# Performance work log

Hardware: AMD Instinct MI355X
Metric: run time of the kernel (lower is better)

The kernel has to match this reference:

```python
import jax, jax.numpy as jnp
import numpy as np

B, L, HID, NH = 1, 2048, 3072, 24
HD = HID // NH          # 128
MLP = HID * 4           # 12288


def _layernorm(x, eps=1e-6):
    # LayerNorm without affine (pre_norm)
    mu = jnp.mean(x, axis=-1, keepdims=True)
    var = jnp.mean(jnp.square(x - mu), axis=-1, keepdims=True)
    return (x - mu) * jax.lax.rsqrt(var + eps)


def _rmsnorm(x, w):
    # torch.nn.RMSNorm with eps=None -> finfo(dtype).eps
    eps = jnp.finfo(x.dtype).eps
    ms = jnp.mean(jnp.square(x), axis=-1, keepdims=True)
    return x * jax.lax.rsqrt(ms + eps) * w


def _apply_rope(x, pe):
    # x: (B, L, H, D); pe: (B, 1, L, D//2, 2, 2)
    b, l, h, d = x.shape
    x_ = x.astype(jnp.float32).reshape(b, l, h, d // 2, 1, 2)
    f = pe[:, :, :, None]                       # (B,1,L,1,D//2,2,2)
    out = f[..., 0] * x_[..., 0] + f[..., 1] * x_[..., 1]
    return out.reshape(b, l, h, d).astype(x.dtype)


def setup_inputs() -> dict:
    key = jax.random.key(0)
    ks = jax.random.split(key, 16)
    s = 0.02
    # pe as proper 2x2 rotation matrices (EmbedND output structure)
    theta = jax.random.uniform(ks[0], (L, HD // 2), minval=0.0, maxval=2.0 * np.pi)
    cos, sin = jnp.cos(theta), jnp.sin(theta)
    rot = jnp.stack([jnp.stack([cos, -sin], -1), jnp.stack([sin, cos], -1)], -2)
    pe = rot[None, None].astype(jnp.float32)    # (1,1,L,HD//2,2,2)
    rnd = lambda k, shp: jax.random.normal(k, shp, jnp.float32)
    return {
        "x": rnd(ks[1], (B, L, HID)),
        "vec": rnd(ks[2], (B, HID)),
        "pe": pe,
        "w_mod": rnd(ks[3], (HID, 3 * HID)) * s,
        "b_mod": rnd(ks[4], (3 * HID,)) * s,
        "w_qkv": rnd(ks[5], (HID, 3 * HID)) * s,
        "b_qkv": rnd(ks[6], (3 * HID,)) * s,
        "w_fc1": rnd(ks[7], (HID, MLP)) * s,
        "b_fc1": rnd(ks[8], (MLP,)) * s,
        "w_fc2": rnd(ks[9], (MLP, HID)) * s,
        "b_fc2": rnd(ks[10], (HID,)) * s,
        "w_out": rnd(ks[11], (HID, HID)) * s,
        "b_out": rnd(ks[12], (HID,)) * s,
        "norm_q_w": jnp.ones((HD,), jnp.float32),
        "norm_k_w": jnp.ones((HD,), jnp.float32),
    }


def reference(x, vec, pe, w_mod, b_mod, w_qkv, b_qkv, w_fc1, b_fc1,
              w_fc2, b_fc2, w_out, b_out, norm_q_w, norm_k_w):
    # modulation: AWQ linear on silu(vec)
    mod = jax.nn.silu(vec) @ w_mod + b_mod            # (B, 3*HID)
    shift, scale, gate = jnp.split(mod[:, None, :], 3, axis=-1)
    x_mod = _layernorm(x) * (1.0 + scale) + shift      # (B, L, HID)

    # qkv projection (SVDQ linear, dequantized math == dense GEMM)
    qkv = x_mod @ w_qkv + b_qkv
    q, k, v = jnp.split(qkv, 3, axis=-1)
    q = _rmsnorm(q.reshape(B, L, NH, HD), norm_q_w)
    k = _rmsnorm(k.reshape(B, L, NH, HD), norm_k_w)
    q = _apply_rope(q, pe)
    k = _apply_rope(k, pe)
    v = v.reshape(B, L, NH, HD)

    # scaled dot-product attention
    scores = jnp.einsum("blhd,bmhd->bhlm", q, k) / jnp.sqrt(jnp.float32(HD))
    probs = jax.nn.softmax(scores, axis=-1)
    attn = jnp.einsum("bhlm,bmhd->blhd", probs, v).reshape(B, L, HID)

    # parallel MLP branch
    mlp = jax.nn.gelu(x_mod @ w_fc1 + b_fc1, approximate=True)
    mlp = mlp @ w_fc2 + b_fc2

    out = attn @ w_out + b_out + mlp
    return x + gate * out
```

## Files before the change

### kernel.cpp

```cpp
#include <hip/hip_runtime.h>
#include <hip/hip_bf16.h>
#include <stdint.h>


typedef __bf16 bf16;
typedef bf16 bf16x2 __attribute__((ext_vector_type(2)));
typedef bf16 bf16x4 __attribute__((ext_vector_type(4)));
typedef bf16 bf16x8 __attribute__((ext_vector_type(8)));
typedef float f32x4 __attribute__((ext_vector_type(4)));

#define L_SEQ 2048
#define HIDD  3072
#define NHH   24
#define HDD   128
#define MLPD  12288
#define N3Q   9216

struct PB { bf16* p[8]; };

__device__ __forceinline__ void gload_lds16(const bf16* g, bf16* l) {
  __builtin_amdgcn_global_load_lds(
      (const __attribute__((address_space(1))) unsigned int*)g,
      (__attribute__((address_space(3))) unsigned int*)l, 16, 0, 0);
}

__device__ __forceinline__ float gelu_tanh(float x) {
  float z = 0.7978845608028654f * (x + 0.044715f * x * x * x);
  float t = 1.f - 2.f / (__expf(2.f * z) + 1.f);
  return 0.5f * x * (1.f + t);
}

__global__ __launch_bounds__(256) void mod_partial(
    const float* __restrict__ vec, const float* __restrict__ w_mod,
    float* __restrict__ part) {
  __shared__ float sv[256];
  int y = blockIdx.y;
  int i0 = y * 256;
  {
    float xv = vec[i0 + threadIdx.x];
    sv[threadIdx.x] = xv / (1.f + __expf(-xv));
  }
  __syncthreads();
  int j = blockIdx.x * 256 + threadIdx.x;
  float acc = 0.f;
#pragma unroll 8
  for (int i = 0; i < 256; ++i)
    acc += sv[i] * w_mod[(size_t)(i0 + i) * N3Q + j];
  part[y * N3Q + j] = acc;
}

__global__ __launch_bounds__(256) void mod_reduce(
    const float* __restrict__ part, const float* __restrict__ b_mod,
    float* __restrict__ mod) {
  int j = blockIdx.x * 256 + threadIdx.x;
  float s = b_mod[j];
#pragma unroll
  for (int p = 0; p < 12; ++p) s += part[p * N3Q + j];
  mod[j] = s;
}

__global__ __launch_bounds__(256) void ln_mod_k(
    const float* __restrict__ x, const float* __restrict__ mod,
    bf16* __restrict__ xm) {
  __shared__ float sb[4];
  int l = blockIdx.x, t = threadIdx.x;
  const float* xr = x + (size_t)l * HIDD;
  float4 v[3];
  float s = 0.f;
#pragma unroll
  for (int p = 0; p < 3; ++p) {
    v[p] = *(const float4*)(xr + p * 1024 + t * 4);
    s += v[p].x + v[p].y + v[p].z + v[p].w;
  }
#pragma unroll
  for (int o = 32; o >= 1; o >>= 1) s += __shfl_xor(s, o);
  if (!(t & 63)) sb[t >> 6] = s;
  __syncthreads();
  float mean = (sb[0] + sb[1] + sb[2] + sb[3]) * (1.f / HIDD);
  __syncthreads();
  float vs = 0.f;
#pragma unroll
  for (int p = 0; p < 3; ++p) {
    float a = v[p].x - mean, b = v[p].y - mean, c = v[p].z - mean,
          d = v[p].w - mean;
    vs += a * a + b * b + c * c + d * d;
  }
#pragma unroll
  for (int o = 32; o >= 1; o >>= 1) vs += __shfl_xor(vs, o);
  if (!(t & 63)) sb[t >> 6] = vs;
  __syncthreads();
  float var = (sb[0] + sb[1] + sb[2] + sb[3]) * (1.f / HIDD);
  float rs = rsqrtf(var + 1e-6f);
#pragma unroll
  for (int p = 0; p < 3; ++p) {
    int j = p * 1024 + t * 4;
    float4 sc = *(const float4*)(mod + HIDD + j);
    float4 sh = *(const float4*)(mod + j);
    bf16x4 o;
    o[0] = (bf16)((v[p].x - mean) * rs * (1.f + sc.x) + sh.x);
    o[1] = (bf16)((v[p].y - mean) * rs * (1.f + sc.y) + sh.y);
    o[2] = (bf16)((v[p].z - mean) * rs * (1.f + sc.z) + sh.z);
    o[3] = (bf16)((v[p].w - mean) * rs * (1.f + sc.w) + sh.w);
    *(bf16x4*)(xm + (size_t)l * HIDD + j) = o;
  }
}

__global__ __launch_bounds__(256) void convT(
    const float* __restrict__ src, bf16* __restrict__ dst, int K, int N) {
  __shared__ bf16 tl[64 * 72];
  int n0 = blockIdx.x * 64, k0 = blockIdx.y * 64;
  int t = threadIdx.x;
#pragma unroll
  for (int p = 0; p < 4; ++p) {
    int idx = p * 256 + t;
    int kr = idx >> 4, c4 = (idx & 15) << 2;
    float4 v = *(const float4*)(src + (size_t)(k0 + kr) * N + n0 + c4);
    bf16x4 b;
    b[0] = (bf16)v.x; b[1] = (bf16)v.y; b[2] = (bf16)v.z; b[3] = (bf16)v.w;
    *(bf16x4*)(tl + kr * 72 + c4) = b;
  }
  __syncthreads();
#pragma unroll
  for (int p = 0; p < 2; ++p) {
    int idx = p * 256 + t;
    int nr = idx >> 3, c = idx & 7;
    bf16x8 o;
#pragma unroll
    for (int j = 0; j < 8; ++j) o[j] = tl[(c * 8 + j) * 72 + nr];
    *(bf16x8*)(dst + (size_t)(n0 + nr) * K + k0 + c * 8) = o;
  }
}

template <int EPI>
__global__ __launch_bounds__(512, 2) void gemm256(
    const bf16* __restrict__ A, const bf16* __restrict__ BT,
    const float* __restrict__ bias, int lda, int klen, int ldc, PB dst,
    bf16* __restrict__ o1) {
  __shared__ bf16 LA[2][2][8192];
  __shared__ bf16 LB[2][2][8192];
  const int tid = threadIdx.x;
  const int w = tid >> 6, lane = tid & 63;
  const int wm = w >> 2, wn = w & 3;
  const int g = lane >> 4, r16 = lane & 15;
  const int row0 = blockIdx.x * 256, col0 = blockIdx.y * 256;
  const size_t kb = (size_t)blockIdx.z * klen;

  const int s_r = tid >> 3, s_c = tid & 7;
  const bf16* gA = A + (size_t)(row0 + s_r) * lda + kb + ((s_c ^ (s_r & 7)) << 3);
  const bf16* gB = BT + (size_t)(col0 + s_r) * lda + kb + ((s_c ^ (s_r & 7)) << 3);
  const int wofs = w * 512;

#define STG_A(buf, h, t)                                                       \
  do {                                                                         \
    gload_lds16(gA + (size_t)((h) * 128) * lda + (t) * 64, &LA[buf][h][wofs]); \
    gload_lds16(gA + (size_t)((h) * 128 + 64) * lda + (t) * 64,                \
                &LA[buf][h][4096 + wofs]);                                     \
  } while (0)
#define STG_B(buf, h, t)                                                       \
  do {                                                                         \
    gload_lds16(gB + (size_t)((h) * 128) * lda + (t) * 64, &LB[buf][h][wofs]); \
    gload_lds16(gB + (size_t)((h) * 128 + 64) * lda + (t) * 64,                \
                &LB[buf][h][4096 + wofs]);                                     \
  } while (0)
#define LGKM0()                                               \
  do {                                                        \
    asm volatile("s_waitcnt lgkmcnt(0)" ::: "memory");        \
    __builtin_amdgcn_sched_barrier(0);                        \
  } while (0)
#define MF(mb, AF, BF)                                                     \
  do {                                                                     \
    __builtin_amdgcn_s_setprio(1);                                         \
    _Pragma("unroll") for (int m_ = 0; m_ < 4; ++m_)                       \
        _Pragma("unroll") for (int n_ = 0; n_ < 4; ++n_)                   \
            acc[(mb) + m_][n_] = __builtin_amdgcn_mfma_f32_16x16x32_bf16(  \
                AF[(mb) + m_], BF[n_], acc[(mb) + m_][n_], 0, 0, 0);       \
    __builtin_amdgcn_s_setprio(0);                                         \
  } while (0)

  f32x4 acc[8][4] = {};
  const int nk = klen >> 6;
  const int swz0 = (g ^ (r16 & 7)) << 3;
  const int swz1 = ((4 + g) ^ (r16 & 7)) << 3;
  const int brow = (wn & 1) * 64;
  const int hb = wn >> 1;

  STG_A(0, 0, 0); STG_A(0, 1, 0); STG_B(0, 0, 0); STG_B(0, 1, 0);
  STG_B(1, 0, 1); STG_A(1, 0, 1); STG_A(1, 1, 1);
  asm volatile("s_waitcnt vmcnt(6)" ::: "memory");
  __builtin_amdgcn_s_barrier();

  for (int t = 0; t < nk; ++t) {
    const int buf = t & 1;
    const bf16* la = LA[buf][wm];
    const bf16* lb = LB[buf][hb];
    bf16x8 af0[8], af1[8], bf0[4], bf1[4];

#pragma unroll
    for (int m = 0; m < 8; ++m)
      af0[m] = *(const bf16x8*)(la + (m * 16 + r16) * 64 + swz0);
#pragma unroll
    for (int n = 0; n < 4; ++n)
      bf0[n] = *(const bf16x8*)(lb + (brow + n * 16 + r16) * 64 + swz0);
    __builtin_amdgcn_s_barrier();
    LGKM0();
    if (t + 1 < nk) STG_B(buf ^ 1, 1, t + 1);
    MF(0, af0, bf0);
    __builtin_amdgcn_s_barrier();

#pragma unroll
    for (int n = 0; n < 4; ++n)
      bf1[n] = *(const bf16x8*)(lb + (brow + n * 16 + r16) * 64 + swz1);
    __builtin_amdgcn_s_barrier();
    LGKM0();
    if (t + 2 < nk) STG_B(buf, 0, t + 2);
    MF(4, af0, bf0);
    __builtin_amdgcn_s_barrier();

#pragma unroll
    for (int m = 0; m < 4; ++m)
      af1[m] = *(const bf16x8*)(la + (m * 16 + r16) * 64 + swz1);
    __builtin_amdgcn_s_barrier();
    LGKM0();
    MF(0, af1, bf1);
    __builtin_amdgcn_s_barrier();

#pragma unroll
    for (int m = 4; m < 8; ++m)
      af1[m] = *(const bf16x8*)(la + (m * 16 + r16) * 64 + swz1);
    __builtin_amdgcn_s_barrier();
    LGKM0();
    if (t + 2 < nk) { STG_A(buf, 0, t + 2); STG_A(buf, 1, t + 2); }
    if (t < nk - 2) {
      asm volatile("s_waitcnt vmcnt(6)" ::: "memory");
    } else if (t == nk - 2) {
      asm volatile("s_waitcnt vmcnt(0)" ::: "memory");
    }
    MF(4, af1, bf1);
    __builtin_amdgcn_s_barrier();
  }
#undef STG_A
#undef STG_B
#undef LGKM0
#undef MF

  bf16* dp = (EPI == 0) ? dst.p[blockIdx.z] : o1;
#pragma unroll
  for (int m = 0; m < 8; ++m) {
    int row = row0 + wm * 128 + m * 16 + g * 4;
#pragma unroll
    for (int n = 0; n < 4; ++n) {
      int col = col0 + wn * 64 + n * 16 + r16;
      float bv = (EPI == 1) ? bias[col] : 0.f;
#pragma unroll
      for (int r = 0; r < 4; ++r) {
        float v = acc[m][n][r] + bv;
        if (EPI == 1) v = gelu_tanh(v);
        dp[(size_t)(row + r) * ldc + col] = (bf16)v;
      }
    }
  }
}

__global__ __launch_bounds__(256) void qknorm_rope_k(
    const bf16* __restrict__ P0, const bf16* __restrict__ P1,
    const float* __restrict__ b_qkv, const float* __restrict__ pe,
    const float* __restrict__ qw, const float* __restrict__ kw,
    bf16* __restrict__ qb, bf16* __restrict__ kb) {
  int t = threadIdx.x, lane = t & 63, w = t >> 6;
  int pair = blockIdx.x * 4 + w;
  int h = pair % NHH, l = pair / NHH;
  size_t qi = (size_t)l * N3Q + h * HDD + 2 * lane;
  size_t ob = (size_t)l * HIDD + h * HDD + 2 * lane;
  float4 f = *(const float4*)(pe + (size_t)l * 256 + lane * 4);
  float2 wq = *(const float2*)(qw + 2 * lane);
  float2 wk = *(const float2*)(kw + 2 * lane);
  {
    bf16x2 a = *(const bf16x2*)(P0 + qi);
    bf16x2 b = *(const bf16x2*)(P1 + qi);
    float2 bq = *(const float2*)(b_qkv + h * HDD + 2 * lane);
    float x0 = (float)a[0] + (float)b[0] + bq.x;
    float x1 = (float)a[1] + (float)b[1] + bq.y;
    float ss = x0 * x0 + x1 * x1;
#pragma unroll
    for (int o = 32; o >= 1; o >>= 1) ss += __shfl_xor(ss, o);
    float rs = rsqrtf(ss * (1.f / HDD) + 1.1920929e-7f);
    x0 *= rs * wq.x; x1 *= rs * wq.y;
    const float qs = 0.08838834764831845f;
    bf16x2 ov;
    ov[0] = (bf16)((f.x * x0 + f.y * x1) * qs);
    ov[1] = (bf16)((f.z * x0 + f.w * x1) * qs);
    *(bf16x2*)(qb + ob) = ov;
  }
  {
    bf16x2 a = *(const bf16x2*)(P0 + qi + HIDD);
    bf16x2 b = *(const bf16x2*)(P1 + qi + HIDD);
    float2 bk = *(const float2*)(b_qkv + HIDD + h * HDD + 2 * lane);
    float x0 = (float)a[0] + (float)b[0] + bk.x;
    float x1 = (float)a[1] + (float)b[1] + bk.y;
    float ss = x0 * x0 + x1 * x1;
#pragma unroll
    for (int o = 32; o >= 1; o >>= 1) ss += __shfl_xor(ss, o);
    float rs = rsqrtf(ss * (1.f / HDD) + 1.1920929e-7f);
    x0 *= rs * wk.x; x1 *= rs * wk.y;
    bf16x2 ov;
    ov[0] = (bf16)(f.x * x0 + f.y * x1);
    ov[1] = (bf16)(f.z * x0 + f.w * x1);
    *(bf16x2*)(kb + ob) = ov;
  }
}

__global__ __launch_bounds__(256) void vtrans_k(
    const bf16* __restrict__ P0, const bf16* __restrict__ P1,
    const float* __restrict__ b_qkv, bf16* __restrict__ vt) {
  __shared__ bf16 tl[128 * 128];
  int t = threadIdx.x, lt = blockIdx.x, h = blockIdx.y;
#pragma unroll
  for (int p = 0; p < 8; ++p) {
    int idx = p * 256 + t;
    int i = idx >> 4, c = idx & 15;
    size_t gi = (size_t)(lt * 128 + i) * N3Q + 2 * HIDD + h * HDD + c * 8;
    bf16x8 a = *(const bf16x8*)(P0 + gi);
    bf16x8 b = *(const bf16x8*)(P1 + gi);
    bf16x8 val;
#pragma unroll
    for (int e = 0; e < 8; ++e)
      val[e] = (bf16)((float)a[e] + (float)b[e] +
                      b_qkv[2 * HIDD + h * HDD + c * 8 + e]);
    *(bf16x8*)(tl + i * 128 + ((c ^ (i & 15)) << 3)) = val;
  }
  __syncthreads();
#pragma unroll
  for (int p = 0; p < 8; ++p) {
    int idx = p * 256 + t;
    int j = idx >> 4, i8 = (idx & 15) << 3;
    bf16x8 o;
#pragma unroll
    for (int e = 0; e < 8; ++e) {
      int row = i8 + e;
      o[e] = tl[row * 128 + ((((j >> 3) ^ (row & 15)) << 3) | (j & 7))];
    }
    *(bf16x8*)(vt + ((size_t)h * HDD + j) * L_SEQ + lt * 128 + i8) = o;
  }
}

__global__ __launch_bounds__(256) void attn_k(
    const bf16* __restrict__ q, const bf16* __restrict__ k,
    const bf16* __restrict__ vt, bf16* __restrict__ out) {
  __shared__ bf16 Ks[64 * 128];
  __shared__ bf16 Vs[128 * 64];
  __shared__ bf16 Ps[4][16 * 72];
  int tid = threadIdx.x, lane = tid & 63, w = tid >> 6;
  int g = lane >> 4, r16 = lane & 15;
  int qt = blockIdx.x, h = blockIdx.y;
  int qbase = qt * 64 + w * 16;

  bf16x8 qreg[4];
  const bf16* qrow = q + (size_t)(qbase + r16) * HIDD + h * HDD;
#pragma unroll
  for (int c = 0; c < 4; ++c) qreg[c] = *(const bf16x8*)(qrow + c * 32 + g * 8);

  f32x4 acc[8] = {};
  float m_run = -3.0e38f, l_run = 0.f;
  bf16* ps = &Ps[w][0];

  for (int kv0 = 0; kv0 < L_SEQ; kv0 += 64) {
    __syncthreads();
#pragma unroll
    for (int p = 0; p < 4; ++p) {
      int ci = p * 256 + tid;
      {
        int rr = ci >> 4, cc = ci & 15;
        gload_lds16(k + (size_t)(kv0 + rr) * HIDD + h * HDD +
                        ((cc ^ (rr & 15)) << 3),
                    Ks + ((p * 4 + w) << 9));
      }
      {
        int rr = ci >> 3, cc = ci & 7;
        gload_lds16(vt + ((size_t)h * HDD + rr) * L_SEQ + kv0 +
                        ((cc ^ (rr & 7)) << 3),
                    Vs + ((p * 4 + w) << 9));
      }
    }
    __syncthreads();

    f32x4 st[4] = {};
#pragma unroll
    for (int m4 = 0; m4 < 4; ++m4) {
#pragma unroll
      for (int c = 0; c < 4; ++c) {
        int rr = m4 * 16 + r16;
        bf16x8 kf =
            *(const bf16x8*)(Ks + rr * 128 + (((c * 4 + g) ^ (rr & 15)) << 3));
        st[m4] =
            __builtin_amdgcn_mfma_f32_16x16x32_bf16(kf, qreg[c], st[m4], 0, 0, 0);
      }
    }
    float cmax = -3.0e38f;
#pragma unroll
    for (int m4 = 0; m4 < 4; ++m4)
#pragma unroll
      for (int r = 0; r < 4; ++r) cmax = fmaxf(cmax, st[m4][r]);
    cmax = fmaxf(cmax, __shfl_xor(cmax, 16));
    cmax = fmaxf(cmax, __shfl_xor(cmax, 32));
    float m_new = fmaxf(m_run, cmax);
    float corr = __expf(m_run - m_new);
    float psum = 0.f;
#pragma unroll
    for (int m4 = 0; m4 < 4; ++m4) {
      bf16x4 pk;
#pragma unroll
      for (int r = 0; r < 4; ++r) {
        float pv = __expf(st[m4][r] - m_new);
        psum += pv;
        pk[r] = (bf16)pv;
      }
      *(bf16x4*)(ps + r16 * 72 + m4 * 16 + g * 4) = pk;
    }
    psum += __shfl_xor(psum, 16);
    psum += __shfl_xor(psum, 32);
    l_run = l_run * corr + psum;
    m_run = m_new;
    float corr_r[4];
#pragma unroll
    for (int r = 0; r < 4; ++r) corr_r[r] = __shfl(corr, g * 4 + r);
#pragma unroll
    for (int nt = 0; nt < 8; ++nt)
#pragma unroll
      for (int r = 0; r < 4; ++r) acc[nt][r] *= corr_r[r];
#pragma unroll
    for (int ks = 0; ks < 2; ++ks) {
      bf16x8 pf = *(const bf16x8*)(ps + r16 * 72 + ks * 32 + g * 8);
#pragma unroll
      for (int nt = 0; nt < 8; ++nt) {
        int rr = nt * 16 + r16;
        bf16x8 vf =
            *(const bf16x8*)(Vs + rr * 64 + (((ks * 4 + g) ^ (rr & 7)) << 3));
        acc[nt] = __builtin_amdgcn_mfma_f32_16x16x32_bf16(pf, vf, acc[nt], 0, 0, 0);
      }
    }
  }
  float inv = 1.f / l_run;
  float inv_r[4];
#pragma unroll
  for (int r = 0; r < 4; ++r) inv_r[r] = __shfl(inv, g * 4 + r);
#pragma unroll
  for (int nt = 0; nt < 8; ++nt)
#pragma unroll
    for (int r = 0; r < 4; ++r)
      out[(size_t)(qbase + g * 4 + r) * HIDD + h * HDD + nt * 16 + r16] =
          (bf16)(acc[nt][r] * inv_r[r]);
}

__global__ __launch_bounds__(256) void osum_k(
    const bf16* __restrict__ a, const bf16* __restrict__ b,
    float* __restrict__ o) {
  size_t i = ((size_t)blockIdx.x * 256 + threadIdx.x) * 4;
  bf16x4 va = *(const bf16x4*)(a + i);
  bf16x4 vb = *(const bf16x4*)(b + i);
  float4 s;
  s.x = (float)va[0] + (float)vb[0];
  s.y = (float)va[1] + (float)vb[1];
  s.z = (float)va[2] + (float)vb[2];
  s.w = (float)va[3] + (float)vb[3];
  *(float4*)(o + i) = s;
}

__global__ __launch_bounds__(256) void final_k(
    const float* __restrict__ x, PB ps, const float* __restrict__ mod,
    const float* __restrict__ b_out, const float* __restrict__ b_fc2,
    float* __restrict__ out) {
  int l = blockIdx.x, t = threadIdx.x;
#pragma unroll
  for (int p = 0; p < 3; ++p) {
    int c = p * 1024 + t * 4;
    size_t idx = (size_t)l * HIDD + c;
    float4 xv = *(const float4*)(x + idx);
    float4 gv = *(const float4*)(mod + 2 * HIDD + c);
    float4 bo = *(const float4*)(b_out + c);
    float4 bf = *(const float4*)(b_fc2 + c);
    float4 da = *(const float4*)(out + idx);
    float a0 = da.x + bo.x + bf.x, a1 = da.y + bo.y + bf.y;
    float a2 = da.z + bo.z + bf.z, a3 = da.w + bo.w + bf.w;
#pragma unroll
    for (int i = 0; i < 8; ++i) {
      bf16x4 v = *(const bf16x4*)(ps.p[i] + idx);
      a0 += (float)v[0]; a1 += (float)v[1];
      a2 += (float)v[2]; a3 += (float)v[3];
    }
    float4 o;
    o.x = xv.x + gv.x * a0;
    o.y = xv.y + gv.y * a1;
    o.z = xv.z + gv.z * a2;
    o.w = xv.w + gv.w * a3;
    *(float4*)(out + idx) = o;
  }
}

extern "C" void kernel_launch(void* const* d_in, const int* in_sizes, int n_in,
                              void* d_out, int out_size, void* d_ws,
                              size_t ws_size, hipStream_t stream) {
  const float* x     = (const float*)d_in[0];
  const float* vec   = (const float*)d_in[1];
  const float* pe    = (const float*)d_in[2];
  const float* w_mod = (const float*)d_in[3];
  const float* b_mod = (const float*)d_in[4];
  const float* w_qkv = (const float*)d_in[5];
  const float* b_qkv = (const float*)d_in[6];
  const float* w_fc1 = (const float*)d_in[7];
  const float* b_fc1 = (const float*)d_in[8];
  const float* w_fc2 = (const float*)d_in[9];
  const float* b_fc2 = (const float*)d_in[10];
  const float* w_out = (const float*)d_in[11];
  const float* b_out = (const float*)d_in[12];
  const float* qw    = (const float*)d_in[13];
  const float* kw    = (const float*)d_in[14];
  float* out = (float*)d_out;

  char* ws = (char*)d_ws;
  float* mod  = (float*)(ws + 0);
  bf16* xmod  = (bf16*)(ws + 36864);
  bf16* qb    = (bf16*)(ws + 12619776);
  bf16* kbuf  = (bf16*)(ws + 25202688);
  bf16* vt    = (bf16*)(ws + 37785600);
  bf16* att   = (bf16*)(ws + 50368512);
  bf16* mlp   = (bf16*)(ws + 62951424);
  bf16* wt    = (bf16*)(ws + 113283072);
  bf16* P0    = (bf16*)(ws + 188780544);
  bf16* P1    = (bf16*)(ws + 62951424);
  float* part = (float*)(ws + 188780544);
  bf16* pO0   = qb;
  bf16* pO1   = kbuf;
  bf16* pF0   = xmod;
  bf16* pF1   = vt;
  bf16* pF2   = att;
  bf16* pF3   = (bf16*)(ws + 188780544);
  bf16* pF4   = (bf16*)(ws + 201363456);
  bf16* pF5   = (bf16*)(ws + 213946368);
  bf16* pF6   = qb;
  bf16* pF7   = kbuf;

  mod_partial<<<dim3(36, 12), 256, 0, stream>>>(vec, w_mod, part);
  mod_reduce<<<36, 256, 0, stream>>>(part, b_mod, mod);
  ln_mod_k<<<2048, 256, 0, stream>>>(x, mod, xmod);

  convT<<<dim3(144, 48), 256, 0, stream>>>(w_qkv, wt, 3072, 9216);
  PB Pq = {}; Pq.p[0] = P0; Pq.p[1] = P1;
  gemm256<0><<<dim3(8, 36, 2), 512, 0, stream>>>(xmod, wt, nullptr, 3072, 1536,
                                                 9216, Pq, nullptr);
  qknorm_rope_k<<<12288, 256, 0, stream>>>(P0, P1, b_qkv, pe, qw, kw, qb, kbuf);
  vtrans_k<<<dim3(16, 24), 256, 0, stream>>>(P0, P1, b_qkv, vt);
  attn_k<<<dim3(32, 24), 256, 0, stream>>>(qb, kbuf, vt, att);

  convT<<<dim3(48, 48), 256, 0, stream>>>(w_out, wt, 3072, 3072);
  PB Po = {}; Po.p[0] = pO0; Po.p[1] = pO1;
  gemm256<0><<<dim3(8, 12, 2), 512, 0, stream>>>(att, wt, nullptr, 3072, 1536,
                                                 3072, Po, nullptr);
  osum_k<<<6144, 256, 0, stream>>>(pO0, pO1, out);

  convT<<<dim3(192, 48), 256, 0, stream>>>(w_fc1, wt, 3072, 12288);
  PB Pz = {};
  gemm256<1><<<dim3(8, 48, 1), 512, 0, stream>>>(xmod, wt, b_fc1, 3072, 3072,
                                                 12288, Pz, mlp);

  convT<<<dim3(48, 192), 256, 0, stream>>>(w_fc2, wt, 12288, 3072);
  PB Pf = {};
  Pf.p[0] = pF0; Pf.p[1] = pF1; Pf.p[2] = pF2; Pf.p[3] = pF3;
  Pf.p[4] = pF4; Pf.p[5] = pF5; Pf.p[6] = pF6; Pf.p[7] = pF7;
  gemm256<0><<<dim3(8, 12, 8), 512, 0, stream>>>(mlp, wt, nullptr, 12288, 1536,
                                                 3072, Pf, nullptr);

  final_k<<<2048, 256, 0, stream>>>(x, Pf, mod, b_out, b_fc2, out);
}
```

Measured before the change: 972.7 us.

## Restructure GEMM k-loop into quadrant MFMA groups, swizzle grid, split-K fc1/out

The GEMM mainloop is rewritten as two unrolled groups per iteration. Each group computes four quadrant MFMA blocks with both k-halves, with reordered LDS reads and global-to-LDS staging to overlap loads with compute. Launches use a 1-D grid remapped through an XCD-style swizzle to improve L2 locality. The fc1 GEMM now uses split-K with a separate sum+bias+GELU kernel, and the out-projection uses 4-way split-K. This raises occupancy on smaller GEMMs at the cost of extra partial-buffer traffic and an additional elementwise kernel.

```diff
diff --git a/kernel.cpp b/kernel.cpp
--- a/kernel.cpp
+++ b/kernel.cpp
@@ -131,19 +131,27 @@
   }
 }
 
-template <int EPI>
 __global__ __launch_bounds__(512, 2) void gemm256(
     const bf16* __restrict__ A, const bf16* __restrict__ BT,
-    const float* __restrict__ bias, int lda, int klen, int ldc, PB dst,
-    bf16* __restrict__ o1) {
+    int lda, int klen, int ldc, int gy, int gz, PB dst) {
   __shared__ bf16 LA[2][2][8192];
   __shared__ bf16 LB[2][2][8192];
   const int tid = threadIdx.x;
   const int w = tid >> 6, lane = tid & 63;
   const int wm = w >> 2, wn = w & 3;
   const int g = lane >> 4, r16 = lane & 15;
-  const int row0 = blockIdx.x * 256, col0 = blockIdx.y * 256;
-  const size_t kb = (size_t)blockIdx.z * klen;
+  const int hb = wn >> 1, brow = (wn & 1) * 64;
+
+  const int nwg = 8 * gy * gz;
+  int id = (int)blockIdx.x;
+  int sw = (id & 7) * (nwg >> 3) + (id >> 3);
+  const int bx = sw & 7;
+  const int rem = sw >> 3;
+  const int by = rem % gy;
+  const int bz = rem / gy;
+
+  const int row0 = bx * 256, col0 = by * 256;
+  const size_t kb = (size_t)bz * klen;
 
   const int s_r = tid >> 3, s_c = tid & 7;
   const bf16* gA = A + (size_t)(row0 + s_r) * lda + kb + ((s_c ^ (s_r & 7)) << 3);
@@ -152,14 +160,16 @@
 
 #define STG_A(buf, h, t)                                                       \
   do {                                                                         \
-    gload_lds16(gA + (size_t)((h) * 128) * lda + (t) * 64, &LA[buf][h][wofs]); \
-    gload_lds16(gA + (size_t)((h) * 128 + 64) * lda + (t) * 64,                \
+    gload_lds16(gA + (size_t)((h) * 128) * lda + (size_t)(t) * 64,             \
+                &LA[buf][h][wofs]);                                            \
+    gload_lds16(gA + (size_t)((h) * 128 + 64) * lda + (size_t)(t) * 64,        \
                 &LA[buf][h][4096 + wofs]);                                     \
   } while (0)
 #define STG_B(buf, h, t)                                                       \
   do {                                                                         \
-    gload_lds16(gB + (size_t)((h) * 128) * lda + (t) * 64, &LB[buf][h][wofs]); \
-    gload_lds16(gB + (size_t)((h) * 128 + 64) * lda + (t) * 64,                \
+    gload_lds16(gB + (size_t)((h) * 128) * lda + (size_t)(t) * 64,             \
+                &LB[buf][h][wofs]);                                            \
+    gload_lds16(gB + (size_t)((h) * 128 + 64) * lda + (size_t)(t) * 64,        \
                 &LB[buf][h][4096 + wofs]);                                     \
   } while (0)
 #define LGKM0()                                               \
@@ -167,96 +177,97 @@
     asm volatile("s_waitcnt lgkmcnt(0)" ::: "memory");        \
     __builtin_amdgcn_sched_barrier(0);                        \
   } while (0)
-#define MF(mb, AF, BF)                                                     \
-  do {                                                                     \
-    __builtin_amdgcn_s_setprio(1);                                         \
-    _Pragma("unroll") for (int m_ = 0; m_ < 4; ++m_)                       \
-        _Pragma("unroll") for (int n_ = 0; n_ < 4; ++n_)                   \
-            acc[(mb) + m_][n_] = __builtin_amdgcn_mfma_f32_16x16x32_bf16(  \
-                AF[(mb) + m_], BF[n_], acc[(mb) + m_][n_], 0, 0, 0);       \
-    __builtin_amdgcn_s_setprio(0);                                         \
+#define RD_A4(DST, LAP, MB)                                                    \
+  _Pragma("unroll") for (int m_ = 0; m_ < 4; ++m_)                             \
+  _Pragma("unroll") for (int kk_ = 0; kk_ < 2; ++kk_)                          \
+      DST[m_][kk_] = *(const bf16x8*)((LAP) + (((MB) + m_) * 16 + r16) * 64 +  \
+                                      (((kk_ * 4 + g) ^ (r16 & 7)) << 3));
+#define RD_B2(DST, LBP, NB)                                                    \
+  _Pragma("unroll") for (int n_ = 0; n_ < 2; ++n_)                             \
+  _Pragma("unroll") for (int kk_ = 0; kk_ < 2; ++kk_)                          \
+      DST[n_][kk_] = *(const bf16x8*)(                                         \
+          (LBP) + (brow + ((NB) + n_) * 16 + r16) * 64 +                       \
+          (((kk_ * 4 + g) ^ (r16 & 7)) << 3));
+#define QUAD(AF, BF, MB, NB)                                                   \
+  do {                                                                         \
+    __builtin_amdgcn_s_setprio(1);                                             \
+    _Pragma("unroll") for (int kk_ = 0; kk_ < 2; ++kk_)                        \
+    _Pragma("unroll") for (int m_ = 0; m_ < 4; ++m_)                           \
+    _Pragma("unroll") for (int n_ = 0; n_ < 2; ++n_)                           \
+        acc[(MB) + m_][(NB) + n_] = __builtin_amdgcn_mfma_f32_16x16x32_bf16(   \
+            AF[m_][kk_], BF[n_][kk_], acc[(MB) + m_][(NB) + n_], 0, 0, 0);     \
+    __builtin_amdgcn_s_setprio(0);                                             \
+  } while (0)
+
+#define GROUP(TB, T1, T2)                                                      \
+  do {                                                                         \
+    const bf16* la = &LA[TB][wm][0];                                           \
+    const bf16* lb = &LB[TB][hb][0];                                           \
+    bf16x8 aL[4][2], aH[4][2], bL[2][2], bH[2][2];                             \
+                                           \
+    RD_A4(aL, la, 0);                                                          \
+    RD_B2(bL, lb, 0);                                                          \
+    if ((T1) < nk) STG_B(TB ^ 1, 1, T1);                                       \
+    asm volatile("s_waitcnt lgkmcnt(8)" ::: "memory");                         \
+    __builtin_amdgcn_s_barrier();                                              \
+    LGKM0();                                                                   \
+    QUAD(aL, bL, 0, 0);                                                        \
+    __builtin_amdgcn_s_barrier();                                              \
+                      \
+    RD_A4(aH, la, 4);                                                          \
+    __builtin_amdgcn_s_barrier();                                              \
+    LGKM0();                                                                   \
+    QUAD(aH, bL, 4, 0);                                                        \
+    __builtin_amdgcn_s_barrier();                                              \
+     \
+    RD_B2(bH, lb, 2);                                                          \
+    if ((T2) < nk) { STG_A(TB, 0, T2); STG_A(TB, 1, T2); }                     \
+    __builtin_amdgcn_s_barrier();                                              \
+    LGKM0();                                                                   \
+    QUAD(aL, bH, 0, 2);                                                        \
+    __builtin_amdgcn_s_barrier();                                              \
+       \
+    if ((T2) < nk) {                                                           \
+      STG_B(TB, 0, T2);                                                        \
+      asm volatile("s_waitcnt vmcnt(6)" ::: "memory");                         \
+    } else {                                                                   \
+      asm volatile("s_waitcnt vmcnt(0)" ::: "memory");                         \
+    }                                                                          \
+    __builtin_amdgcn_s_barrier();                                              \
+    QUAD(aH, bH, 4, 2);                                                        \
+    __builtin_amdgcn_s_barrier();                                              \
   } while (0)
 
   f32x4 acc[8][4] = {};
   const int nk = klen >> 6;
-  const int swz0 = (g ^ (r16 & 7)) << 3;
-  const int swz1 = ((4 + g) ^ (r16 & 7)) << 3;
-  const int brow = (wn & 1) * 64;
-  const int hb = wn >> 1;
 
   STG_A(0, 0, 0); STG_A(0, 1, 0); STG_B(0, 0, 0); STG_B(0, 1, 0);
-  STG_B(1, 0, 1); STG_A(1, 0, 1); STG_A(1, 1, 1);
+  STG_A(1, 0, 1); STG_A(1, 1, 1); STG_B(1, 0, 1);
   asm volatile("s_waitcnt vmcnt(6)" ::: "memory");
   __builtin_amdgcn_s_barrier();
 
-  for (int t = 0; t < nk; ++t) {
-    const int buf = t & 1;
-    const bf16* la = LA[buf][wm];
-    const bf16* lb = LB[buf][hb];
-    bf16x8 af0[8], af1[8], bf0[4], bf1[4];
-
-#pragma unroll
-    for (int m = 0; m < 8; ++m)
-      af0[m] = *(const bf16x8*)(la + (m * 16 + r16) * 64 + swz0);
-#pragma unroll
-    for (int n = 0; n < 4; ++n)
-      bf0[n] = *(const bf16x8*)(lb + (brow + n * 16 + r16) * 64 + swz0);
-    __builtin_amdgcn_s_barrier();
-    LGKM0();
-    if (t + 1 < nk) STG_B(buf ^ 1, 1, t + 1);
-    MF(0, af0, bf0);
-    __builtin_amdgcn_s_barrier();
-
-#pragma unroll
-    for (int n = 0; n < 4; ++n)
-      bf1[n] = *(const bf16x8*)(lb + (brow + n * 16 + r16) * 64 + swz1);
-    __builtin_amdgcn_s_barrier();
-    LGKM0();
-    if (t + 2 < nk) STG_B(buf, 0, t + 2);
-    MF(4, af0, bf0);
-    __builtin_amdgcn_s_barrier();
-
-#pragma unroll
-    for (int m = 0; m < 4; ++m)
-      af1[m] = *(const bf16x8*)(la + (m * 16 + r16) * 64 + swz1);
-    __builtin_amdgcn_s_barrier();
-    LGKM0();
-    MF(0, af1, bf1);
-    __builtin_amdgcn_s_barrier();
-
-#pragma unroll
-    for (int m = 4; m < 8; ++m)
-      af1[m] = *(const bf16x8*)(la + (m * 16 + r16) * 64 + swz1);
-    __builtin_amdgcn_s_barrier();
-    LGKM0();
-    if (t + 2 < nk) { STG_A(buf, 0, t + 2); STG_A(buf, 1, t + 2); }
-    if (t < nk - 2) {
-      asm volatile("s_waitcnt vmcnt(6)" ::: "memory");
-    } else if (t == nk - 2) {
-      asm volatile("s_waitcnt vmcnt(0)" ::: "memory");
-    }
-    MF(4, af1, bf1);
-    __builtin_amdgcn_s_barrier();
+  for (int t = 0; t < nk; t += 2) {
+    GROUP(0, t + 1, t + 2);
+    GROUP(1, t + 2, t + 3);
   }
 #undef STG_A
 #undef STG_B
 #undef LGKM0
-#undef MF
-
-  bf16* dp = (EPI == 0) ? dst.p[blockIdx.z] : o1;
+#undef RD_A4
+#undef RD_B2
+#undef QUAD
+#undef GROUP
+
+  bf16* dp = dst.p[bz];
 #pragma unroll
   for (int m = 0; m < 8; ++m) {
     int row = row0 + wm * 128 + m * 16 + g * 4;
 #pragma unroll
     for (int n = 0; n < 4; ++n) {
       int col = col0 + wn * 64 + n * 16 + r16;
-      float bv = (EPI == 1) ? bias[col] : 0.f;
-#pragma unroll
-      for (int r = 0; r < 4; ++r) {
-        float v = acc[m][n][r] + bv;
-        if (EPI == 1) v = gelu_tanh(v);
-        dp[(size_t)(row + r) * ldc + col] = (bf16)v;
-      }
+#pragma unroll
+      for (int r = 0; r < 4; ++r)
+        dp[(size_t)(row + r) * ldc + col] = (bf16)acc[m][n][r];
     }
   }
 }
@@ -453,16 +464,36 @@
 
 __global__ __launch_bounds__(256) void osum_k(
     const bf16* __restrict__ a, const bf16* __restrict__ b,
+    const bf16* __restrict__ c, const bf16* __restrict__ d,
     float* __restrict__ o) {
   size_t i = ((size_t)blockIdx.x * 256 + threadIdx.x) * 4;
   bf16x4 va = *(const bf16x4*)(a + i);
   bf16x4 vb = *(const bf16x4*)(b + i);
+  bf16x4 vc = *(const bf16x4*)(c + i);
+  bf16x4 vd = *(const bf16x4*)(d + i);
   float4 s;
-  s.x = (float)va[0] + (float)vb[0];
-  s.y = (float)va[1] + (float)vb[1];
-  s.z = (float)va[2] + (float)vb[2];
-  s.w = (float)va[3] + (float)vb[3];
+  s.x = (float)va[0] + (float)vb[0] + (float)vc[0] + (float)vd[0];
+  s.y = (float)va[1] + (float)vb[1] + (float)vc[1] + (float)vd[1];
+  s.z = (float)va[2] + (float)vb[2] + (float)vc[2] + (float)vd[2];
+  s.w = (float)va[3] + (float)vb[3] + (float)vc[3] + (float)vd[3];
   *(float4*)(o + i) = s;
+}
+
+__global__ __launch_bounds__(256) void sumgelu_k(
+    const bf16* __restrict__ p0, const bf16* __restrict__ p1,
+    const float* __restrict__ b, bf16* __restrict__ o) {
+  size_t i = ((size_t)blockIdx.x * 256 + threadIdx.x) * 8;
+  int col = (int)(i % MLPD);
+  bf16x8 a = *(const bf16x8*)(p0 + i);
+  bf16x8 c = *(const bf16x8*)(p1 + i);
+  float4 b0 = *(const float4*)(b + col);
+  float4 b1 = *(const float4*)(b + col + 4);
+  float bb[8] = {b0.x, b0.y, b0.z, b0.w, b1.x, b1.y, b1.z, b1.w};
+  bf16x8 o8;
+#pragma unroll
+  for (int j = 0; j < 8; ++j)
+    o8[j] = (bf16)gelu_tanh((float)a[j] + (float)c[j] + bb[j]);
+  *(bf16x8*)(o + i) = o8;
 }
 
 __global__ __launch_bounds__(256) void final_k(
@@ -518,26 +549,18 @@
 
   char* ws = (char*)d_ws;
   float* mod  = (float*)(ws + 0);
-  bf16* xmod  = (bf16*)(ws + 36864);
-  bf16* qb    = (bf16*)(ws + 12619776);
-  bf16* kbuf  = (bf16*)(ws + 25202688);
-  bf16* vt    = (bf16*)(ws + 37785600);
-  bf16* att   = (bf16*)(ws + 50368512);
-  bf16* mlp   = (bf16*)(ws + 62951424);
-  bf16* wt    = (bf16*)(ws + 113283072);
-  bf16* P0    = (bf16*)(ws + 188780544);
-  bf16* P1    = (bf16*)(ws + 62951424);
-  float* part = (float*)(ws + 188780544);
-  bf16* pO0   = qb;
-  bf16* pO1   = kbuf;
-  bf16* pF0   = xmod;
-  bf16* pF1   = vt;
-  bf16* pF2   = att;
-  bf16* pF3   = (bf16*)(ws + 188780544);
-  bf16* pF4   = (bf16*)(ws + 201363456);
-  bf16* pF5   = (bf16*)(ws + 213946368);
-  bf16* pF6   = qb;
-  bf16* pF7   = kbuf;
+  bf16* xmod  = (bf16*)(ws + 65536);
+  bf16* qb    = (bf16*)(ws + 12648448);
+  bf16* kbuf  = (bf16*)(ws + 25231360);
+  bf16* vt    = (bf16*)(ws + 37814272);
+  bf16* att   = (bf16*)(ws + 50397184);
+  bf16* mlpF  = (bf16*)(ws + 62980096);
+  bf16* wt    = (bf16*)(ws + 113311744);
+  bf16* P0    = (bf16*)(ws + 188809216);
+  float* part = (float*)(ws + 188809216);
+  bf16* P1    = mlpF;
+  bf16* H1    = (bf16*)(ws + 188809216 + 12582912);
+  bf16* H2    = (bf16*)(ws + 188809216 + 25165824);
 
   mod_partial<<<dim3(36, 12), 256, 0, stream>>>(vec, w_mod, part);
   mod_reduce<<<36, 256, 0, stream>>>(part, b_mod, mod);
@@ -545,29 +568,26 @@
 
   convT<<<dim3(144, 48), 256, 0, stream>>>(w_qkv, wt, 3072, 9216);
   PB Pq = {}; Pq.p[0] = P0; Pq.p[1] = P1;
-  gemm256<0><<<dim3(8, 36, 2), 512, 0, stream>>>(xmod, wt, nullptr, 3072, 1536,
-                                                 9216, Pq, nullptr);
+  gemm256<<<576, 512, 0, stream>>>(xmod, wt, 3072, 1536, 9216, 36, 2, Pq);
   qknorm_rope_k<<<12288, 256, 0, stream>>>(P0, P1, b_qkv, pe, qw, kw, qb, kbuf);
   vtrans_k<<<dim3(16, 24), 256, 0, stream>>>(P0, P1, b_qkv, vt);
   attn_k<<<dim3(32, 24), 256, 0, stream>>>(qb, kbuf, vt, att);
 
   convT<<<dim3(48, 48), 256, 0, stream>>>(w_out, wt, 3072, 3072);
-  PB Po = {}; Po.p[0] = pO0; Po.p[1] = pO1;
-  gemm256<0><<<dim3(8, 12, 2), 512, 0, stream>>>(att, wt, nullptr, 3072, 1536,
-                                                 3072, Po, nullptr);
-  osum_k<<<6144, 256, 0, stream>>>(pO0, pO1, out);
+  PB Po = {}; Po.p[0] = qb; Po.p[1] = kbuf; Po.p[2] = vt; Po.p[3] = P0;
+  gemm256<<<384, 512, 0, stream>>>(att, wt, 3072, 768, 3072, 12, 4, Po);
+  osum_k<<<6144, 256, 0, stream>>>(qb, kbuf, vt, P0, out);
 
   convT<<<dim3(192, 48), 256, 0, stream>>>(w_fc1, wt, 3072, 12288);
-  PB Pz = {};
-  gemm256<1><<<dim3(8, 48, 1), 512, 0, stream>>>(xmod, wt, b_fc1, 3072, 3072,
-                                                 12288, Pz, mlp);
+  PB Pg = {}; Pg.p[0] = mlpF; Pg.p[1] = qb;
+  gemm256<<<768, 512, 0, stream>>>(xmod, wt, 3072, 1536, 12288, 48, 2, Pg);
+  sumgelu_k<<<12288, 256, 0, stream>>>(mlpF, qb, b_fc1, mlpF);
 
   convT<<<dim3(48, 192), 256, 0, stream>>>(w_fc2, wt, 12288, 3072);
   PB Pf = {};
-  Pf.p[0] = pF0; Pf.p[1] = pF1; Pf.p[2] = pF2; Pf.p[3] = pF3;
-  Pf.p[4] = pF4; Pf.p[5] = pF5; Pf.p[6] = pF6; Pf.p[7] = pF7;
-  gemm256<0><<<dim3(8, 12, 8), 512, 0, stream>>>(mlp, wt, nullptr, 12288, 1536,
-                                                 3072, Pf, nullptr);
+  Pf.p[0] = xmod; Pf.p[1] = qb; Pf.p[2] = kbuf; Pf.p[3] = vt;
+  Pf.p[4] = att;  Pf.p[5] = P0; Pf.p[6] = H1;   Pf.p[7] = H2;
+  gemm256<<<768, 512, 0, stream>>>(mlpF, wt, 12288, 1536, 3072, 12, 8, Pf);
 
   final_k<<<2048, 256, 0, stream>>>(x, Pf, mod, b_out, b_fc2, out);
 }
```

Result: faster. 888.0 us (-8.7%).
